# Kernel optimization log

Hardware: AMD Instinct MI355X
Metric: run time of the kernel (lower is better)

The kernel has to match this reference:

```python
import jax, jax.numpy as jnp
import numpy as np

N, n, d = 4, 2048, 1024


def setup_inputs() -> dict:
    key = jax.random.key(0)
    k1, k2, k3, k4 = jax.random.split(key, 4)
    x = jax.random.normal(k1, (N, n, d), dtype=jnp.float32)
    mask = jax.random.randint(k2, (N, n, n), 0, 2, dtype=jnp.int32)
    Wqk = jax.random.normal(k3, (d, d), dtype=jnp.float32) * (d ** -0.5)
    Wvc = jax.random.normal(k4, (d, d), dtype=jnp.float32) * (d ** -0.5)
    return {"x": x, "mask": mask, "Wqk": Wqk, "Wvc": Wvc}


def reference(x, mask, Wqk, Wvc):
    # q = Wqk(x): torch Linear computes x @ W^T
    q = jnp.einsum('bnd,ed->bne', x, Wqk)          # [N, n, d]
    scale = jnp.asarray(x.shape[-1], x.dtype) ** 0.5
    scores = jnp.einsum('bnd,bmd->bnm', q, x) / scale  # [N, n, n]
    scores = jnp.where(mask == 0, jnp.asarray(-1e20, scores.dtype), scores)
    attention = jax.nn.softmax(scores, axis=-1)
    attended = jnp.einsum('bnm,bmd->bnd', attention, x)
    return jnp.einsum('bnd,ed->bne', attended, Wvc)
```

## Files before the change

kernel.cpp:

```cpp
#include <hip/hip_runtime.h>
#include <hip/hip_bf16.h>

typedef short bf16x8 __attribute__((ext_vector_type(8)));
typedef short s16x4  __attribute__((ext_vector_type(4)));
typedef short s16x8  __attribute__((ext_vector_type(8)));
typedef float f32x4  __attribute__((ext_vector_type(4)));

static __device__ __forceinline__ void async_cp16(const void* g, void* l) {
  __builtin_amdgcn_global_load_lds(
      (const __attribute__((address_space(1))) unsigned int*)g,
      (__attribute__((address_space(3))) unsigned int*)l, 16, 0, 0);
}

static __device__ __forceinline__ unsigned short f2bf_bits(float f) {
  union { __hip_bfloat16 b; unsigned short u; } cv;
  cv.b = __float2bfloat16(f);
  return cv.u;
}
static __device__ __forceinline__ float bf2f(short u) {
  union { float f; unsigned v; } cv;
  cv.v = ((unsigned)(unsigned short)u) << 16;
  return cv.f;
}

#define BAR() __builtin_amdgcn_s_barrier()
#define SBZ() __builtin_amdgcn_sched_barrier(0)
#define LGKM0() do { asm volatile("s_waitcnt lgkmcnt(0)" ::: "memory"); SBZ(); } while (0)
#define VMW(n) do { asm volatile("s_waitcnt vmcnt(" #n ")" ::: "memory"); SBZ(); } while (0)

__global__ __launch_bounds__(256) void cvt_all(const float* __restrict__ x,
                                               const float* __restrict__ wqk,
                                               const float* __restrict__ wvc,
                                               __hip_bfloat16* __restrict__ xb,
                                               __hip_bfloat16* __restrict__ wqkb,
                                               __hip_bfloat16* __restrict__ wvcb) {
  const int b = blockIdx.x;
  const float* in;
  __hip_bfloat16* out;
  long base;
  if (b < 8192)       { in = x;   out = xb;   base = (long)b * 1024; }
  else if (b < 9216)  { in = wqk; out = wqkb; base = (long)(b - 8192) * 1024; }
  else                { in = wvc; out = wvcb; base = (long)(b - 9216) * 1024; }
  const long i = base + threadIdx.x * 4;
  const float4 v = *(const float4*)(in + i);
  s16x4 o;
  o[0] = (short)f2bf_bits(v.x);
  o[1] = (short)f2bf_bits(v.y);
  o[2] = (short)f2bf_bits(v.z);
  o[3] = (short)f2bf_bits(v.w);
  *(s16x4*)(out + i) = o;
}

struct GemmDesc {
  const __hip_bfloat16* A; const __hip_bfloat16* B; void* C;
  int lda, ldb, ldc, nT, tpb; long sA, sB, sC; float cscale;
};

template<int MODE>
__global__ __launch_bounds__(512, 2) void gemm8p(GemmDesc g0, GemmDesc g1, int nb0, int K) {
  __shared__ char lds[131072];
  const int bid = blockIdx.x, nwg = gridDim.x;
  const int wg = (bid & 7) * (nwg >> 3) + (bid >> 3);
  GemmDesc g = (wg < nb0) ? g0 : g1;
  const int id = (wg < nb0) ? wg : wg - nb0;
  const int bz = id / g.tpb, tl = id - bz * g.tpb;
  const int bm = tl / g.nT, bn = tl - bm * g.nT;
  const long m0 = (long)bm * 256, n0 = (long)bn * 256;
  const __hip_bfloat16* Ab = g.A + bz * g.sA;
  const __hip_bfloat16* Bb = g.B + bz * g.sB;

  const int t = threadIdx.x, lane = t & 63, w = t >> 6;
  const int wm = w >> 2, wn = w & 3;
  const int lr = lane & 15, cs = lane >> 4;

  const int srow = t >> 3;
  const int sslot = (t & 7) ^ (srow & 7);
  const __hip_bfloat16* aP[2][2];
  const __hip_bfloat16* bP[2][2];
  #pragma unroll
  for (int h = 0; h < 2; ++h)
    #pragma unroll
    for (int i = 0; i < 2; ++i) {
      aP[h][i] = Ab + (m0 + h * 128 + i * 64 + srow) * g.lda + sslot * 8;
      bP[h][i] = Bb + (n0 + h * 128 + i * 64 + srow) * g.ldb + sslot * 8;
    }

  int aOf[8], bOf[4];
  #pragma unroll
  for (int mm = 0; mm < 8; ++mm)
    aOf[mm] = wm * 16384 + (mm * 16 + lr) * 128 + ((cs ^ (lr & 7)) << 4);
  #pragma unroll
  for (int nf = 0; nf < 4; ++nf)
    bOf[nf] = 32768 + (wn >> 1) * 16384 + ((wn & 1) * 64 + nf * 16 + lr) * 128 +
              ((cs ^ (lr & 7)) << 4);

  f32x4 acc[8][4] = {};
  bf16x8 af[4][2], bqA[2][2], bqB[2][2];

  #define STG(P, h, kt, dbase) do { \
    async_cp16(P[h][0] + (long)(kt) * 64, lds + (dbase) + t * 16); \
    async_cp16(P[h][1] + (long)(kt) * 64, lds + (dbase) + 8192 + t * 16); } while (0)
  #define RD_AF(mb, bufb) do { _Pragma("unroll") for (int mm_ = 0; mm_ < 4; ++mm_) { \
      af[mm_][0] = *(const bf16x8*)(lds + (bufb) + aOf[(mb) * 4 + mm_]); \
      af[mm_][1] = *(const bf16x8*)(lds + (bufb) + (aOf[(mb) * 4 + mm_] ^ 64)); } } while (0)
  #define RD_BQ(dst, nb, bufb) do { _Pragma("unroll") for (int nf_ = 0; nf_ < 2; ++nf_) { \
      dst[nf_][0] = *(const bf16x8*)(lds + (bufb) + bOf[(nb) * 2 + nf_]); \
      dst[nf_][1] = *(const bf16x8*)(lds + (bufb) + (bOf[(nb) * 2 + nf_] ^ 64)); } } while (0)
  #define MM16(BQ, NB, MB) do { \
    __builtin_amdgcn_s_setprio(1); \
    _Pragma("unroll") for (int ks_ = 0; ks_ < 2; ++ks_) \
      _Pragma("unroll") for (int mm_ = 0; mm_ < 4; ++mm_) \
        _Pragma("unroll") for (int nf_ = 0; nf_ < 2; ++nf_) \
          acc[(MB) + mm_][(NB) + nf_] = __builtin_amdgcn_mfma_f32_16x16x32_bf16( \
              af[mm_][ks_], BQ[nf_][ks_], acc[(MB) + mm_][(NB) + nf_], 0, 0, 0); \
    __builtin_amdgcn_s_setprio(0); } while (0)

  const int nt = K >> 6, nJ = nt >> 1;
  STG(bP, 0, 0, 32768); STG(bP, 1, 0, 49152);
  STG(aP, 0, 0, 0);     STG(aP, 1, 0, 16384);
  STG(bP, 0, 1, 65536 + 32768); STG(bP, 1, 1, 65536 + 49152);
  VMW(4);
  BAR(); SBZ();

  for (int j = 0; j < nJ; ++j) {
    const bool full = (j + 1 < nJ);
    const int tb = 2 * j + 1, ta2 = 2 * j + 2, tb2 = 2 * j + 3;
    RD_AF(0, 0); RD_BQ(bqA, 0, 0);
    STG(aP, 0, tb, 65536);
    LGKM0();
    MM16(bqA, 0, 0);
    BAR(); SBZ();
    RD_BQ(bqB, 1, 0);
    STG(aP, 1, tb, 65536 + 16384);
    LGKM0();
    MM16(bqB, 2, 0);
    BAR(); SBZ();
    RD_AF(1, 0);
    if (full) STG(bP, 0, ta2, 32768);
    LGKM0();
    MM16(bqB, 2, 4);
    BAR(); SBZ();
    if (full) STG(bP, 1, ta2, 49152);
    MM16(bqA, 0, 4);
    if (full) { VMW(4); } else { VMW(0); }
    BAR(); SBZ();
    RD_AF(0, 65536); RD_BQ(bqA, 0, 65536);
    if (full) STG(aP, 0, ta2, 0);
    LGKM0();
    MM16(bqA, 0, 0);
    BAR(); SBZ();
    RD_BQ(bqB, 1, 65536);
    if (full) STG(aP, 1, ta2, 16384);
    LGKM0();
    MM16(bqB, 2, 0);
    BAR(); SBZ();
    RD_AF(1, 65536);
    if (full) STG(bP, 0, tb2, 65536 + 32768);
    LGKM0();
    MM16(bqB, 2, 4);
    BAR(); SBZ();
    if (full) STG(bP, 1, tb2, 65536 + 49152);
    MM16(bqA, 0, 4);
    if (full) { VMW(4); } else { VMW(0); }
    BAR(); SBZ();
  }
  #undef STG
  #undef RD_AF
  #undef RD_BQ
  #undef MM16

  const long crow0 = m0 + wm * 128 + cs * 4;
  const long ccol0 = n0 + wn * 64 + lr;
  if (MODE == 0) {
    float* C = (float*)g.C + bz * g.sC;
    #pragma unroll
    for (int mm = 0; mm < 8; ++mm)
      #pragma unroll
      for (int nf = 0; nf < 4; ++nf)
        #pragma unroll
        for (int rr = 0; rr < 4; ++rr)
          C[(crow0 + mm * 16 + rr) * g.ldc + ccol0 + nf * 16] = acc[mm][nf][rr];
  } else {
    __hip_bfloat16* C = (__hip_bfloat16*)g.C + bz * g.sC;
    #pragma unroll
    for (int mm = 0; mm < 8; ++mm)
      #pragma unroll
      for (int nf = 0; nf < 4; ++nf)
        #pragma unroll
        for (int rr = 0; rr < 4; ++rr)
          C[(crow0 + mm * 16 + rr) * g.ldc + ccol0 + nf * 16] =
              __float2bfloat16(acc[mm][nf][rr] * g.cscale);
  }
}

template<int MODE, int BM_, int BK_>
__global__ __launch_bounds__(1024, 4) void gemm16(GemmDesc g0, GemmDesc g1, int nb0, int K) {
  constexpr int MR = BM_ / 64;
  constexpr int KR = BK_ / 32;
  constexpr int W  = BK_ * 2;
  constexpr int NB = (256 * W) / 16384;
  constexpr int BUFSZ = 16384 + NB * 16384;
  constexpr int KW = 1 + NB;
  __shared__ char lds[3 * BUFSZ];

  const int bid = blockIdx.x, nwg = gridDim.x;
  const int wg = (bid & 7) * (nwg >> 3) + (bid >> 3);
  GemmDesc g = (wg < nb0) ? g0 : g1;
  const int id = (wg < nb0) ? wg : wg - nb0;
  const int bz = id / g.tpb, tl = id - bz * g.tpb;
  const int bm = tl / g.nT, bn = tl - bm * g.nT;
  const long m0 = (long)bm * BM_, n0 = (long)bn * 256;
  const __hip_bfloat16* Ab = g.A + bz * g.sA;
  const __hip_bfloat16* Bb = g.B + bz * g.sB;

  const int t = threadIdx.x;
  const int lane = t & 63, w = t >> 6;
  const int wm = w >> 2, wn = w & 3;
  const int lr = lane & 15, cs = lane >> 4;

  const int rA  = t / (W / 16);
  const int dsl = t % (W / 16);
  const int ssl = dsl ^ ((W == 64) ? ((rA >> 1) & 3) : (rA & 7));
  const __hip_bfloat16* aSt  = Ab + (m0 + rA) * g.lda + ssl * 8;
  const __hip_bfloat16* bSt0 = Bb + (n0 + rA) * g.ldb + ssl * 8;
  const __hip_bfloat16* bSt1 = Bb + (n0 + 128 + rA) * g.ldb + ssl * 8;

  const int axor = (W == 64) ? (((lr >> 1) & 3) << 4) : ((lr & 7) << 4);
  int aRd[MR][KR], bRd[4][KR];
  #pragma unroll
  for (int mm = 0; mm < MR; ++mm)
    #pragma unroll
    for (int ks = 0; ks < KR; ++ks)
      aRd[mm][ks] = (wm * (BM_ / 4) + mm * 16 + lr) * W + ((((ks * 4 + cs) << 4) ^ axor));
  #pragma unroll
  for (int nf = 0; nf < 4; ++nf)
    #pragma unroll
    for (int ks = 0; ks < KR; ++ks)
      bRd[nf][ks] = 16384 + (wn * 64 + nf * 16 + lr) * W + ((((ks * 4 + cs) << 4) ^ axor));

  f32x4 acc[MR][4] = {};

  #define STAGE(kt, base) do { \
    async_cp16(aSt + (long)(kt) * BK_, lds + (base) + t * 16); \
    async_cp16(bSt0 + (long)(kt) * BK_, lds + (base) + 16384 + t * 16); \
    if (NB == 2) async_cp16(bSt1 + (long)(kt) * BK_, lds + (base) + 32768 + t * 16); \
  } while (0)
  #define VM_KW() do { if constexpr (KW == 2) { VMW(2); } else { VMW(3); } } while (0)

  const int nt = K / BK_;
  STAGE(0, 0);
  STAGE(1, BUFSZ);
  VM_KW();
  BAR();

  int rb = 0, sb = 2 * BUFSZ;
  for (int tt = 0; tt < nt; ++tt) {
    bf16x8 af[MR][KR], bq[4][KR];
    #pragma unroll
    for (int mm = 0; mm < MR; ++mm)
      #pragma unroll
      for (int ks = 0; ks < KR; ++ks)
        af[mm][ks] = *(const bf16x8*)(lds + rb + aRd[mm][ks]);
    #pragma unroll
    for (int nf = 0; nf < 4; ++nf)
      #pragma unroll
      for (int ks = 0; ks < KR; ++ks)
        bq[nf][ks] = *(const bf16x8*)(lds + rb + bRd[nf][ks]);
    if (tt + 2 < nt) STAGE(tt + 2, sb);
    #pragma unroll
    for (int ks = 0; ks < KR; ++ks)
      #pragma unroll
      for (int mm = 0; mm < MR; ++mm)
        #pragma unroll
        for (int nf = 0; nf < 4; ++nf)
          acc[mm][nf] = __builtin_amdgcn_mfma_f32_16x16x32_bf16(af[mm][ks], bq[nf][ks], acc[mm][nf], 0, 0, 0);
    if (tt + 2 < nt) { VM_KW(); } else { VMW(0); }
    BAR();
    rb = (rb == 2 * BUFSZ) ? 0 : rb + BUFSZ;
    sb = (sb == 2 * BUFSZ) ? 0 : sb + BUFSZ;
  }
  #undef STAGE
  #undef VM_KW

  const long crow0 = m0 + wm * (BM_ / 4) + cs * 4;
  const long ccol0 = n0 + wn * 64 + lr;
  if (MODE == 0) {
    float* C = (float*)g.C + bz * g.sC;
    #pragma unroll
    for (int mm = 0; mm < MR; ++mm)
      #pragma unroll
      for (int nf = 0; nf < 4; ++nf)
        #pragma unroll
        for (int rr = 0; rr < 4; ++rr)
          C[(crow0 + mm * 16 + rr) * g.ldc + ccol0 + nf * 16] = acc[mm][nf][rr];
  } else {
    __hip_bfloat16* C = (__hip_bfloat16*)g.C + bz * g.sC;
    #pragma unroll
    for (int mm = 0; mm < MR; ++mm)
      #pragma unroll
      for (int nf = 0; nf < 4; ++nf)
        #pragma unroll
        for (int rr = 0; rr < 4; ++rr)
          C[(crow0 + mm * 16 + rr) * g.ldc + ccol0 + nf * 16] =
              __float2bfloat16(acc[mm][nf][rr] * g.cscale);
  }
}

__global__ __launch_bounds__(256) void softmax_rows(__hip_bfloat16* __restrict__ S,
                                                    const int* __restrict__ Mask) {
  const long row = blockIdx.x;
  short* srow = (short*)(S + row * 2048);
  const int* mrow = Mask + row * 2048;
  const int t = threadIdx.x;
  const s16x8 sv = *(const s16x8*)(srow + t * 8);
  const int4 q0 = *(const int4*)(mrow + t * 8);
  const int4 q1 = *(const int4*)(mrow + t * 8 + 4);
  const int mk[8] = {q0.x, q0.y, q0.z, q0.w, q1.x, q1.y, q1.z, q1.w};

  float e[8];
  float s = 0.f;
  #pragma unroll
  for (int i = 0; i < 8; ++i) {
    e[i] = mk[i] ? __expf(bf2f(sv[i])) : 0.f;
    s += e[i];
  }
  #pragma unroll
  for (int off = 32; off > 0; off >>= 1) s += __shfl_xor(s, off);
  __shared__ float reds[4];
  if ((t & 63) == 0) reds[t >> 6] = s;
  __syncthreads();
  s = reds[0] + reds[1] + reds[2] + reds[3];

  s16x8 o;
  if (s > 0.f) {
    const float inv = 1.f / s;
    #pragma unroll
    for (int i = 0; i < 8; ++i) o[i] = (short)f2bf_bits(e[i] * inv);
  } else {
    const unsigned short u = f2bf_bits(1.f / 2048.f);
    #pragma unroll
    for (int i = 0; i < 8; ++i) o[i] = (short)u;
  }
  *(s16x8*)(srow + t * 8) = o;
}

extern "C" void kernel_launch(void* const* d_in, const int* in_sizes, int n_in,
                              void* d_out, int out_size, void* d_ws, size_t ws_size,
                              hipStream_t stream) {
  const float* x   = (const float*)d_in[0];
  const int*   msk = (const int*)d_in[1];
  const float* Wqk = (const float*)d_in[2];
  const float* Wvc = (const float*)d_in[3];
  float* out = (float*)d_out;
  char* ws = (char*)d_ws;

  __hip_bfloat16* xb   = (__hip_bfloat16*)(ws + 0);
  __hip_bfloat16* qb   = (__hip_bfloat16*)(ws + 16777216);
  __hip_bfloat16* vT   = (__hip_bfloat16*)(ws + 33554432);
  __hip_bfloat16* wqkb = (__hip_bfloat16*)(ws + 50331648);
  __hip_bfloat16* wvcb = (__hip_bfloat16*)(ws + 52428800);
  __hip_bfloat16* Sbf  = (__hip_bfloat16*)(ws + 54525952);

  cvt_all<<<dim3(10240), 256, 0, stream>>>(x, Wqk, Wvc, xb, wqkb, wvcb);

  GemmDesc gq{xb,   wqkb, qb, 1024, 1024, 1024, 4, 128, 0L, 0L, 0L, 0.03125f};
  GemmDesc gv{wvcb, xb,   vT, 1024, 1024, 2048, 8, 32, 0L, 2097152L, 2097152L, 1.f};
  gemm8p<1><<<dim3(256), 512, 0, stream>>>(gq, gv, 128, 1024);

  GemmDesc gs{qb, xb, Sbf, 1024, 1024, 2048, 8, 64, 2097152L, 2097152L, 4194304L, 1.f};
  gemm8p<1><<<dim3(256), 512, 0, stream>>>(gs, gs, 256, 1024);

  softmax_rows<<<dim3(8192), 256, 0, stream>>>(Sbf, msk);

  GemmDesc go{Sbf, vT, out, 2048, 2048, 1024, 4, 64, 4194304L, 2097152L, 2097152L, 1.f};
  gemm16<0, 128, 64><<<dim3(256), 1024, 0, stream>>>(go, go, 256, 2048);
}
```

Before: 139.0 us.

## Replace ping-pong GEMM pipeline with four-buffer K=32 async staging ring

Swaps the hand-interleaved two-buffer K=64 GEMM schedule for a simpler ring of four K=32 LDS buffers, keeping three tiles in flight. Each iteration reads the whole A/B fragment set, issues the next async stage, then runs 32 MFMAs followed by a single barrier. The LDS swizzle changes to fit 64-byte rows. This is meant to hide global-load latency with deeper prefetch and fewer barriers per tile. In exchange it drops the explicit priority hints and the fine-grained LDS-read/MFMA interleaving, and it keeps more fragment registers live at once.

```diff
diff --git a/kernel.cpp b/kernel.cpp
--- a/kernel.cpp
+++ b/kernel.cpp
@@ -25,7 +25,6 @@
 
 #define BAR() __builtin_amdgcn_s_barrier()
 #define SBZ() __builtin_amdgcn_sched_barrier(0)
-#define LGKM0() do { asm volatile("s_waitcnt lgkmcnt(0)" ::: "memory"); SBZ(); } while (0)
 #define VMW(n) do { asm volatile("s_waitcnt vmcnt(" #n ")" ::: "memory"); SBZ(); } while (0)
 
 __global__ __launch_bounds__(256) void cvt_all(const float* __restrict__ x,
@@ -57,8 +56,11 @@
 };
 
 template<int MODE>
-__global__ __launch_bounds__(512, 2) void gemm8p(GemmDesc g0, GemmDesc g1, int nb0, int K) {
-  __shared__ char lds[131072];
+__global__ __launch_bounds__(512, 2) void gemm4b(GemmDesc g0, GemmDesc g1, int nb0, int K) {
+  constexpr int BOFF  = 16384;
+  constexpr int BUFSZ = 32768;
+  __shared__ char lds[4 * BUFSZ];
+
   const int bid = blockIdx.x, nwg = gridDim.x;
   const int wg = (bid & 7) * (nwg >> 3) + (bid >> 3);
   GemmDesc g = (wg < nb0) ? g0 : g1;
@@ -69,105 +71,65 @@
   const __hip_bfloat16* Ab = g.A + bz * g.sA;
   const __hip_bfloat16* Bb = g.B + bz * g.sB;
 
-  const int t = threadIdx.x, lane = t & 63, w = t >> 6;
+  const int t = threadIdx.x;
+  const int lane = t & 63, w = t >> 6;
   const int wm = w >> 2, wn = w & 3;
   const int lr = lane & 15, cs = lane >> 4;
 
-  const int srow = t >> 3;
-  const int sslot = (t & 7) ^ (srow & 7);
-  const __hip_bfloat16* aP[2][2];
-  const __hip_bfloat16* bP[2][2];
-  #pragma unroll
-  for (int h = 0; h < 2; ++h)
-    #pragma unroll
-    for (int i = 0; i < 2; ++i) {
-      aP[h][i] = Ab + (m0 + h * 128 + i * 64 + srow) * g.lda + sslot * 8;
-      bP[h][i] = Bb + (n0 + h * 128 + i * 64 + srow) * g.ldb + sslot * 8;
-    }
-
-  int aOf[8], bOf[4];
+  const int rA  = t >> 2;
+  const int dsl = t & 3;
+  const int ssl = dsl ^ ((rA >> 1) & 3);
+  const __hip_bfloat16* aSt0 = Ab + (m0 + rA) * g.lda + ssl * 8;
+  const __hip_bfloat16* aSt1 = Ab + (m0 + 128 + rA) * g.lda + ssl * 8;
+  const __hip_bfloat16* bSt0 = Bb + (n0 + rA) * g.ldb + ssl * 8;
+  const __hip_bfloat16* bSt1 = Bb + (n0 + 128 + rA) * g.ldb + ssl * 8;
+
+  const int axor = ((lr >> 1) & 3) << 4;
+  int aRd[8], bRd[4];
   #pragma unroll
   for (int mm = 0; mm < 8; ++mm)
-    aOf[mm] = wm * 16384 + (mm * 16 + lr) * 128 + ((cs ^ (lr & 7)) << 4);
+    aRd[mm] = (wm * 128 + mm * 16 + lr) * 64 + ((cs << 4) ^ axor);
   #pragma unroll
   for (int nf = 0; nf < 4; ++nf)
-    bOf[nf] = 32768 + (wn >> 1) * 16384 + ((wn & 1) * 64 + nf * 16 + lr) * 128 +
-              ((cs ^ (lr & 7)) << 4);
+    bRd[nf] = BOFF + (wn * 64 + nf * 16 + lr) * 64 + ((cs << 4) ^ axor);
 
   f32x4 acc[8][4] = {};
-  bf16x8 af[4][2], bqA[2][2], bqB[2][2];
-
-  #define STG(P, h, kt, dbase) do { \
-    async_cp16(P[h][0] + (long)(kt) * 64, lds + (dbase) + t * 16); \
-    async_cp16(P[h][1] + (long)(kt) * 64, lds + (dbase) + 8192 + t * 16); } while (0)
-  #define RD_AF(mb, bufb) do { _Pragma("unroll") for (int mm_ = 0; mm_ < 4; ++mm_) { \
-      af[mm_][0] = *(const bf16x8*)(lds + (bufb) + aOf[(mb) * 4 + mm_]); \
-      af[mm_][1] = *(const bf16x8*)(lds + (bufb) + (aOf[(mb) * 4 + mm_] ^ 64)); } } while (0)
-  #define RD_BQ(dst, nb, bufb) do { _Pragma("unroll") for (int nf_ = 0; nf_ < 2; ++nf_) { \
-      dst[nf_][0] = *(const bf16x8*)(lds + (bufb) + bOf[(nb) * 2 + nf_]); \
-      dst[nf_][1] = *(const bf16x8*)(lds + (bufb) + (bOf[(nb) * 2 + nf_] ^ 64)); } } while (0)
-  #define MM16(BQ, NB, MB) do { \
-    __builtin_amdgcn_s_setprio(1); \
-    _Pragma("unroll") for (int ks_ = 0; ks_ < 2; ++ks_) \
-      _Pragma("unroll") for (int mm_ = 0; mm_ < 4; ++mm_) \
-        _Pragma("unroll") for (int nf_ = 0; nf_ < 2; ++nf_) \
-          acc[(MB) + mm_][(NB) + nf_] = __builtin_amdgcn_mfma_f32_16x16x32_bf16( \
-              af[mm_][ks_], BQ[nf_][ks_], acc[(MB) + mm_][(NB) + nf_], 0, 0, 0); \
-    __builtin_amdgcn_s_setprio(0); } while (0)
-
-  const int nt = K >> 6, nJ = nt >> 1;
-  STG(bP, 0, 0, 32768); STG(bP, 1, 0, 49152);
-  STG(aP, 0, 0, 0);     STG(aP, 1, 0, 16384);
-  STG(bP, 0, 1, 65536 + 32768); STG(bP, 1, 1, 65536 + 49152);
-  VMW(4);
-  BAR(); SBZ();
-
-  for (int j = 0; j < nJ; ++j) {
-    const bool full = (j + 1 < nJ);
-    const int tb = 2 * j + 1, ta2 = 2 * j + 2, tb2 = 2 * j + 3;
-    RD_AF(0, 0); RD_BQ(bqA, 0, 0);
-    STG(aP, 0, tb, 65536);
-    LGKM0();
-    MM16(bqA, 0, 0);
-    BAR(); SBZ();
-    RD_BQ(bqB, 1, 0);
-    STG(aP, 1, tb, 65536 + 16384);
-    LGKM0();
-    MM16(bqB, 2, 0);
-    BAR(); SBZ();
-    RD_AF(1, 0);
-    if (full) STG(bP, 0, ta2, 32768);
-    LGKM0();
-    MM16(bqB, 2, 4);
-    BAR(); SBZ();
-    if (full) STG(bP, 1, ta2, 49152);
-    MM16(bqA, 0, 4);
-    if (full) { VMW(4); } else { VMW(0); }
-    BAR(); SBZ();
-    RD_AF(0, 65536); RD_BQ(bqA, 0, 65536);
-    if (full) STG(aP, 0, ta2, 0);
-    LGKM0();
-    MM16(bqA, 0, 0);
-    BAR(); SBZ();
-    RD_BQ(bqB, 1, 65536);
-    if (full) STG(aP, 1, ta2, 16384);
-    LGKM0();
-    MM16(bqB, 2, 0);
-    BAR(); SBZ();
-    RD_AF(1, 65536);
-    if (full) STG(bP, 0, tb2, 65536 + 32768);
-    LGKM0();
-    MM16(bqB, 2, 4);
-    BAR(); SBZ();
-    if (full) STG(bP, 1, tb2, 65536 + 49152);
-    MM16(bqA, 0, 4);
-    if (full) { VMW(4); } else { VMW(0); }
-    BAR(); SBZ();
-  }
-  #undef STG
-  #undef RD_AF
-  #undef RD_BQ
-  #undef MM16
+
+  #define STAGE(kt, base) do { \
+    async_cp16(aSt0 + (long)(kt) * 32, lds + (base) + t * 16); \
+    async_cp16(aSt1 + (long)(kt) * 32, lds + (base) + 8192 + t * 16); \
+    async_cp16(bSt0 + (long)(kt) * 32, lds + (base) + BOFF + t * 16); \
+    async_cp16(bSt1 + (long)(kt) * 32, lds + (base) + BOFF + 8192 + t * 16); \
+  } while (0)
+
+  const int nt = K >> 5;
+  STAGE(0, 0);
+  STAGE(1, BUFSZ);
+  STAGE(2, 2 * BUFSZ);
+  VMW(8);
+  BAR();
+
+  int rb = 0, sb = 3 * BUFSZ;
+  for (int tt = 0; tt < nt; ++tt) {
+    bf16x8 af[8], bq[4];
+    #pragma unroll
+    for (int mm = 0; mm < 8; ++mm)
+      af[mm] = *(const bf16x8*)(lds + rb + aRd[mm]);
+    #pragma unroll
+    for (int nf = 0; nf < 4; ++nf)
+      bq[nf] = *(const bf16x8*)(lds + rb + bRd[nf]);
+    if (tt + 3 < nt) STAGE(tt + 3, sb);
+    #pragma unroll
+    for (int mm = 0; mm < 8; ++mm)
+      #pragma unroll
+      for (int nf = 0; nf < 4; ++nf)
+        acc[mm][nf] = __builtin_amdgcn_mfma_f32_16x16x32_bf16(af[mm], bq[nf], acc[mm][nf], 0, 0, 0);
+    if (tt + 3 < nt) { VMW(8); } else { VMW(0); }
+    BAR();
+    rb = (rb == 3 * BUFSZ) ? 0 : rb + BUFSZ;
+    sb = (sb == 3 * BUFSZ) ? 0 : sb + BUFSZ;
+  }
+  #undef STAGE
 
   const long crow0 = m0 + wm * 128 + cs * 4;
   const long ccol0 = n0 + wn * 64 + lr;
@@ -365,10 +327,10 @@
 
   GemmDesc gq{xb,   wqkb, qb, 1024, 1024, 1024, 4, 128, 0L, 0L, 0L, 0.03125f};
   GemmDesc gv{wvcb, xb,   vT, 1024, 1024, 2048, 8, 32, 0L, 2097152L, 2097152L, 1.f};
-  gemm8p<1><<<dim3(256), 512, 0, stream>>>(gq, gv, 128, 1024);
+  gemm4b<1><<<dim3(256), 512, 0, stream>>>(gq, gv, 128, 1024);
 
   GemmDesc gs{qb, xb, Sbf, 1024, 1024, 2048, 8, 64, 2097152L, 2097152L, 4194304L, 1.f};
-  gemm8p<1><<<dim3(256), 512, 0, stream>>>(gs, gs, 256, 1024);
+  gemm4b<1><<<dim3(256), 512, 0, stream>>>(gs, gs, 256, 1024);
 
   softmax_rows<<<dim3(8192), 256, 0, stream>>>(Sbf, msk);
 
```

Measured after the change: 141.5 us. Within noise of the previous version (+1.8%).

## Reschedule 8-wave GEMM pipeline with finer A-tile split and relaxed waits

Applied to the files above, without the earlier changes.

The 256x256 GEMM kernel now splits A-tile staging by row halves so each half-tile load can be issued earlier. The prefetch order is rotated so more loads are in flight (vmcnt 6 instead of 4). Full lgkmcnt(0) waits after each LDS read burst are replaced with partial waits plus extra barriers, and the sched_barrier after each wait is removed. The goal is more overlap of global-to-LDS copies with MFMA work, at the cost of extra barriers and a riskier hand-tuned buffer-hazard schedule.

```diff
diff --git a/kernel.cpp b/kernel.cpp
--- a/kernel.cpp
+++ b/kernel.cpp
@@ -25,8 +25,8 @@
 
 #define BAR() __builtin_amdgcn_s_barrier()
 #define SBZ() __builtin_amdgcn_sched_barrier(0)
-#define LGKM0() do { asm volatile("s_waitcnt lgkmcnt(0)" ::: "memory"); SBZ(); } while (0)
-#define VMW(n) do { asm volatile("s_waitcnt vmcnt(" #n ")" ::: "memory"); SBZ(); } while (0)
+#define LGKM(n) asm volatile("s_waitcnt lgkmcnt(" #n ")" ::: "memory")
+#define VMW(n) asm volatile("s_waitcnt vmcnt(" #n ")" ::: "memory")
 
 __global__ __launch_bounds__(256) void cvt_all(const float* __restrict__ x,
                                                const float* __restrict__ wqk,
@@ -57,7 +57,7 @@
 };
 
 template<int MODE>
-__global__ __launch_bounds__(512, 2) void gemm8p(GemmDesc g0, GemmDesc g1, int nb0, int K) {
+__global__ __launch_bounds__(512, 2) void gemm8t(GemmDesc g0, GemmDesc g1, int nb0, int K) {
   __shared__ char lds[131072];
   const int bid = blockIdx.x, nwg = gridDim.x;
   const int wg = (bid & 7) * (nwg >> 3) + (bid >> 3);
@@ -81,14 +81,15 @@
   for (int h = 0; h < 2; ++h)
     #pragma unroll
     for (int i = 0; i < 2; ++i) {
-      aP[h][i] = Ab + (m0 + h * 128 + i * 64 + srow) * g.lda + sslot * 8;
+      aP[h][i] = Ab + (m0 + i * 128 + h * 64 + srow) * g.lda + sslot * 8;
       bP[h][i] = Bb + (n0 + h * 128 + i * 64 + srow) * g.ldb + sslot * 8;
     }
 
   int aOf[8], bOf[4];
   #pragma unroll
   for (int mm = 0; mm < 8; ++mm)
-    aOf[mm] = wm * 16384 + (mm * 16 + lr) * 128 + ((cs ^ (lr & 7)) << 4);
+    aOf[mm] = (mm >> 2) * 16384 + wm * 8192 + ((mm & 3) * 16 + lr) * 128 +
+              ((cs ^ (lr & 7)) << 4);
   #pragma unroll
   for (int nf = 0; nf < 4; ++nf)
     bOf[nf] = 32768 + (wn >> 1) * 16384 + ((wn & 1) * 64 + nf * 16 + lr) * 128 +
@@ -116,52 +117,57 @@
     __builtin_amdgcn_s_setprio(0); } while (0)
 
   const int nt = K >> 6, nJ = nt >> 1;
-  STG(bP, 0, 0, 32768); STG(bP, 1, 0, 49152);
-  STG(aP, 0, 0, 0);     STG(aP, 1, 0, 16384);
-  STG(bP, 0, 1, 65536 + 32768); STG(bP, 1, 1, 65536 + 49152);
-  VMW(4);
+  STG(aP, 0, 0, 0);     STG(bP, 0, 0, 32768);
+  STG(bP, 1, 0, 49152); STG(aP, 1, 0, 16384);
+  STG(aP, 0, 1, 65536); STG(bP, 0, 1, 65536 + 32768); STG(bP, 1, 1, 65536 + 49152);
+  VMW(6);
   BAR(); SBZ();
 
   for (int j = 0; j < nJ; ++j) {
     const bool full = (j + 1 < nJ);
     const int tb = 2 * j + 1, ta2 = 2 * j + 2, tb2 = 2 * j + 3;
     RD_AF(0, 0); RD_BQ(bqA, 0, 0);
-    STG(aP, 0, tb, 65536);
-    LGKM0();
+    STG(aP, 1, tb, 65536 + 16384);
+    LGKM(8);
+    BAR(); LGKM(0);
     MM16(bqA, 0, 0);
-    BAR(); SBZ();
+    BAR();
     RD_BQ(bqB, 1, 0);
-    STG(aP, 1, tb, 65536 + 16384);
-    LGKM0();
+    if (full) STG(aP, 0, ta2, 0);
+    BAR(); LGKM(0);
     MM16(bqB, 2, 0);
-    BAR(); SBZ();
+    BAR();
     RD_AF(1, 0);
     if (full) STG(bP, 0, ta2, 32768);
-    LGKM0();
+    BAR(); LGKM(0);
     MM16(bqB, 2, 4);
-    BAR(); SBZ();
+    BAR();
     if (full) STG(bP, 1, ta2, 49152);
+    BAR();
     MM16(bqA, 0, 4);
-    if (full) { VMW(4); } else { VMW(0); }
+    if (full) { VMW(6); } else { VMW(2); }
     BAR(); SBZ();
     RD_AF(0, 65536); RD_BQ(bqA, 0, 65536);
-    if (full) STG(aP, 0, ta2, 0);
-    LGKM0();
+    if (full) STG(aP, 1, ta2, 16384);
+    LGKM(8);
+    BAR(); LGKM(0);
     MM16(bqA, 0, 0);
-    BAR(); SBZ();
+    BAR();
     RD_BQ(bqB, 1, 65536);
-    if (full) STG(aP, 1, ta2, 16384);
-    LGKM0();
+    if (full) STG(aP, 0, tb2, 65536);
+    BAR(); LGKM(0);
     MM16(bqB, 2, 0);
-    BAR(); SBZ();
+    if (!full) VMW(0);
+    BAR();
     RD_AF(1, 65536);
     if (full) STG(bP, 0, tb2, 65536 + 32768);
-    LGKM0();
+    BAR(); LGKM(0);
     MM16(bqB, 2, 4);
-    BAR(); SBZ();
+    BAR();
     if (full) STG(bP, 1, tb2, 65536 + 49152);
+    BAR();
     MM16(bqA, 0, 4);
-    if (full) { VMW(4); } else { VMW(0); }
+    if (full) { VMW(6); }
     BAR(); SBZ();
   }
   #undef STG
@@ -245,7 +251,7 @@
     async_cp16(bSt0 + (long)(kt) * BK_, lds + (base) + 16384 + t * 16); \
     if (NB == 2) async_cp16(bSt1 + (long)(kt) * BK_, lds + (base) + 32768 + t * 16); \
   } while (0)
-  #define VM_KW() do { if constexpr (KW == 2) { VMW(2); } else { VMW(3); } } while (0)
+  #define VM_KW() do { if constexpr (KW == 2) { VMW(2); } else { VMW(3); } SBZ(); } while (0)
 
   const int nt = K / BK_;
   STAGE(0, 0);
@@ -274,7 +280,7 @@
         #pragma unroll
         for (int nf = 0; nf < 4; ++nf)
           acc[mm][nf] = __builtin_amdgcn_mfma_f32_16x16x32_bf16(af[mm][ks], bq[nf][ks], acc[mm][nf], 0, 0, 0);
-    if (tt + 2 < nt) { VM_KW(); } else { VMW(0); }
+    if (tt + 2 < nt) { VM_KW(); } else { VMW(0); SBZ(); }
     BAR();
     rb = (rb == 2 * BUFSZ) ? 0 : rb + BUFSZ;
     sb = (sb == 2 * BUFSZ) ? 0 : sb + BUFSZ;
@@ -365,10 +371,10 @@
 
   GemmDesc gq{xb,   wqkb, qb, 1024, 1024, 1024, 4, 128, 0L, 0L, 0L, 0.03125f};
   GemmDesc gv{wvcb, xb,   vT, 1024, 1024, 2048, 8, 32, 0L, 2097152L, 2097152L, 1.f};
-  gemm8p<1><<<dim3(256), 512, 0, stream>>>(gq, gv, 128, 1024);
+  gemm8t<1><<<dim3(256), 512, 0, stream>>>(gq, gv, 128, 1024);
 
   GemmDesc gs{qb, xb, Sbf, 1024, 1024, 2048, 8, 64, 2097152L, 2097152L, 4194304L, 1.f};
-  gemm8p<1><<<dim3(256), 512, 0, stream>>>(gs, gs, 256, 1024);
+  gemm8t<1><<<dim3(256), 512, 0, stream>>>(gs, gs, 256, 1024);
 
   softmax_rows<<<dim3(8192), 256, 0, stream>>>(Sbf, msk);
 
```

Result: slower. 142.2 us (+2.3%).
